# Optimization experiments

Hardware: AMD Instinct MI355X
Metric: run time of the kernel (lower is better)

## Reference

```python
import jax, jax.numpy as jnp
import numpy as np

TOP_K = 8


def setup_inputs() -> dict:
    key = jax.random.key(0)
    k1, k2 = jax.random.split(key)
    hidden_states = jax.random.normal(k1, (4, 4096, 4096), dtype=jnp.float32)
    weight = jax.random.normal(k2, (64, 4096), dtype=jnp.float32) * 0.02
    return {"hidden_states": hidden_states, "weight": weight}


def reference(hidden_states, weight):
    # Flatten [B, S, H] -> [T, H]; gating math is done in float32 (matches .float()).
    h = hidden_states.shape[-1]
    x = hidden_states.reshape(-1, h).astype(jnp.float32)
    # Router logits: [T, E] = [T, H] @ [H, E]
    logits = jnp.einsum('th,eh->te', x, weight.astype(jnp.float32))
    scores = jax.nn.softmax(logits, axis=-1)
    # Top-k expert selection (greedy router)
    topk_weight, topk_idx = jax.lax.top_k(scores, TOP_K)  # [T, K], [T, K]
    # Normalize top-k probabilities (norm_topk_prob=True)
    denom = jnp.sum(topk_weight, axis=-1, keepdims=True) + 1e-20
    topk_weight = topk_weight / denom
    return topk_weight, topk_idx
```

## Files before the change

kernel.cpp:

```cpp
#include <hip/hip_runtime.h>
#include <math.h>

typedef float  f32x4  __attribute__((ext_vector_type(4)));
typedef int    i32x4  __attribute__((ext_vector_type(4)));

#define H      4096
#define E      64
#define TOPK   8
#define TILE_T 32
#define CK     256
#define MS     4
#define NCH    16

__global__ __launch_bounds__(256)
void prep_w(const float* __restrict__ Wg, signed char* __restrict__ Wb)
{
  int n = blockIdx.x * 256 + threadIdx.x;
  int kgrp = n & 3, m = (n >> 2) & 63, e = n >> 8;
  const float* wp = Wg + e * 4096 + m * 64 + kgrp * 16;
  signed char lb[5][16];
  #pragma unroll
  for (int s = 0; s < 16; ++s) {
    long long v = (long long)rint((double)wp[s] * 2199023255552.0);
    #pragma unroll
    for (int j = 0; j < 4; ++j) {
      signed char b = (signed char)(v & 0xff);
      lb[j][s] = b;
      v = (v - b) >> 8;
    }
    lb[4][s] = (signed char)v;
  }
  int lanei = (kgrp << 4) | (e & 15);
  int eq = e >> 4;
  #pragma unroll
  for (int j = 0; j < 5; ++j) {
    i32x4 d;
    #pragma unroll
    for (int r = 0; r < 4; ++r)
      d[r] = (lb[j][4*r] & 0xFF) | ((lb[j][4*r+1] & 0xFF) << 8)
           | ((lb[j][4*r+2] & 0xFF) << 16) | ((lb[j][4*r+3] & 0xFF) << 24);
    *(i32x4*)(Wb + (((size_t)(m * 4 + eq) * 5 + j) << 10) + lanei * 16) = d;
  }
}

__global__ __launch_bounds__(64)
void comp_w(const float* __restrict__ Wg, double* __restrict__ compT)
{
  int e = blockIdx.x;
  int lane = threadIdx.x;
  double s = 0.0;
  #pragma unroll 4
  for (int i = 0; i < 64; ++i)
    s += rint((double)Wg[e * 4096 + i * 64 + lane] * 2199023255552.0);
  #pragma unroll
  for (int off = 32; off >= 1; off >>= 1)
    s += __shfl_xor(s, off);
  if (lane == 0) compT[e] = 8421504.0 * s;
}

__global__ __launch_bounds__(256)
void moe_gate_i8(const float* __restrict__ X, const signed char* __restrict__ Wb,
                 const double* __restrict__ compT, float* __restrict__ out,
                 int n_tokens)
{
  __shared__ char sm[65536];
  double* Ls = (double*)sm;

  const int tid  = threadIdx.x;
  const int lane = tid & 63;
  const int w    = tid >> 6;
  const int t0   = blockIdx.x * TILE_T;
  const int l15  = lane & 15;
  const int kg   = lane >> 4;
  const int dA   = l15 & 7;

  i32x4 z = {0, 0, 0, 0};
  int lab = l15 * 0x01010101;
  i32x4 onev = {0x01010101, 0x01010101, 0x01010101, 0x01010101};
  i32x4 labv = {lab, lab, lab, lab};
  i32x4 pr = __builtin_amdgcn_mfma_i32_16x16x64_i8(labv, onev, z, 0, 0, 0);
  i32x4 pc = __builtin_amdgcn_mfma_i32_16x16x64_i8(onev, labv, z, 0, 0, 0);
  int qrow[4], qcol[4];
  #pragma unroll
  for (int r = 0; r < 4; ++r) { qrow[r] = pr[r] >> 6; qcol[r] = pc[r] >> 6; }

  i32x4 aA3 = z, aA4 = z, aA5 = z, aA6 = z, aA7 = z;
  i32x4 aB3 = z, aB4 = z, aB5 = z, aB6 = z, aB7 = z;

  const signed char* bpp = Wb + w * 5120 + lane * 16;

  #define STAGE(c_, buf_)                                                     \
  {                                                                           \
    _Pragma("unroll")                                                         \
    for (int q = 0; q < 8; ++q) {                                             \
      const int tok_ = w * 8 + q;                                             \
      const float* src_ = X + (size_t)(t0 + tok_) * H + (c_) * CK             \
                            + ((lane ^ (tok_ & 7)) << 2);                     \
      char* dst_ = sm + ((buf_) << 15) + (tok_ << 10);                        \
      __builtin_amdgcn_global_load_lds(                                       \
          (const __attribute__((address_space(1))) void*)src_,                \
          (__attribute__((address_space(3))) void*)dst_, 16, 0, 0);           \
    }                                                                         \
  }

  #define CONV4(xv, W0, W1, W2, W3)                                           \
  {                                                                           \
    unsigned w32[16];                                                         \
    _Pragma("unroll")                                                         \
    for (int r = 0; r < 4; ++r) {                                             \
      f32x4 t_ = xv[r];                                                       \
      _Pragma("unroll")                                                       \
      for (int jj = 0; jj < 4; ++jj)                                          \
        w32[r*4+jj] = ((unsigned)(int)(t_[jj] * 268435456.0f)) ^ 0x00808080u; \
    }                                                                         \
    _Pragma("unroll")                                                         \
    for (int r = 0; r < 4; ++r) {                                             \
      unsigned u0 = w32[4*r], u1 = w32[4*r+1], u2 = w32[4*r+2], u3 = w32[4*r+3];\
      unsigned p01, p23;                                                      \
      p01 = __builtin_amdgcn_perm(u1, u0, 0x04000400u);                       \
      p23 = __builtin_amdgcn_perm(u3, u2, 0x04000400u);                       \
      W0[r] = (int)__builtin_amdgcn_perm(p23, p01, 0x05040100u);              \
      p01 = __builtin_amdgcn_perm(u1, u0, 0x05010501u);                       \
      p23 = __builtin_amdgcn_perm(u3, u2, 0x05010501u);                       \
      W1[r] = (int)__builtin_amdgcn_perm(p23, p01, 0x05040100u);              \
      p01 = __builtin_amdgcn_perm(u1, u0, 0x06020602u);                       \
      p23 = __builtin_amdgcn_perm(u3, u2, 0x06020602u);                       \
      W2[r] = (int)__builtin_amdgcn_perm(p23, p01, 0x05040100u);              \
      p01 = __builtin_amdgcn_perm(u1, u0, 0x07030703u);                       \
      p23 = __builtin_amdgcn_perm(u3, u2, 0x07030703u);                       \
      W3[r] = (int)__builtin_amdgcn_perm(p23, p01, 0x05040100u);              \
    }                                                                         \
  }

  STAGE(0, 0);
  __syncthreads();

  for (int c = 0; c < NCH; ++c) {
    const int cur = c & 1;

    i32x4 bf[4][5];
    #pragma unroll
    for (int m = 0; m < MS; ++m)
      #pragma unroll
      for (int j = 0; j < 5; ++j)
        bf[m][j] = *(const i32x4*)(bpp + (size_t)m * 20480 + (j << 10));
    bpp += (size_t)MS * 20480;

    if (c < NCH - 1) STAGE(c + 1, cur ^ 1);

    const char* base = sm + (cur << 15);
    #pragma unroll
    for (int m = 0; m < MS; ++m) {
      f32x4 va[4], vb[4];
      #pragma unroll
      for (int j = 0; j < 4; ++j) {
        const int slot = ((m * 16 + kg * 4 + j) ^ dA) << 4;
        va[j] = *(const f32x4*)(base + (l15 << 10) + slot);
        vb[j] = *(const f32x4*)(base + ((l15 + 16) << 10) + slot);
      }
      i32x4 xA0, xA1, xA2, xA3, xB0, xB1, xB2, xB3;
      CONV4(va, xA0, xA1, xA2, xA3);
      CONV4(vb, xB0, xB1, xB2, xB3);
      i32x4 b0 = bf[m][0], b1 = bf[m][1], b2 = bf[m][2], b3 = bf[m][3], b4 = bf[m][4];
      aA3 = __builtin_amdgcn_mfma_i32_16x16x64_i8(xA0, b3, aA3, 0, 0, 0);
      aB3 = __builtin_amdgcn_mfma_i32_16x16x64_i8(xB0, b3, aB3, 0, 0, 0);
      aA4 = __builtin_amdgcn_mfma_i32_16x16x64_i8(xA0, b4, aA4, 0, 0, 0);
      aB4 = __builtin_amdgcn_mfma_i32_16x16x64_i8(xB0, b4, aB4, 0, 0, 0);
      aA5 = __builtin_amdgcn_mfma_i32_16x16x64_i8(xA1, b4, aA5, 0, 0, 0);
      aB5 = __builtin_amdgcn_mfma_i32_16x16x64_i8(xB1, b4, aB5, 0, 0, 0);
      aA6 = __builtin_amdgcn_mfma_i32_16x16x64_i8(xA2, b4, aA6, 0, 0, 0);
      aB6 = __builtin_amdgcn_mfma_i32_16x16x64_i8(xB2, b4, aB6, 0, 0, 0);
      aA7 = __builtin_amdgcn_mfma_i32_16x16x64_i8(xA3, b4, aA7, 0, 0, 0);
      aB7 = __builtin_amdgcn_mfma_i32_16x16x64_i8(xB3, b4, aB7, 0, 0, 0);
      aA3 = __builtin_amdgcn_mfma_i32_16x16x64_i8(xA1, b2, aA3, 0, 0, 0);
      aB3 = __builtin_amdgcn_mfma_i32_16x16x64_i8(xB1, b2, aB3, 0, 0, 0);
      aA4 = __builtin_amdgcn_mfma_i32_16x16x64_i8(xA1, b3, aA4, 0, 0, 0);
      aB4 = __builtin_amdgcn_mfma_i32_16x16x64_i8(xB1, b3, aB4, 0, 0, 0);
      aA5 = __builtin_amdgcn_mfma_i32_16x16x64_i8(xA2, b3, aA5, 0, 0, 0);
      aB5 = __builtin_amdgcn_mfma_i32_16x16x64_i8(xB2, b3, aB5, 0, 0, 0);
      aA6 = __builtin_amdgcn_mfma_i32_16x16x64_i8(xA3, b3, aA6, 0, 0, 0);
      aB6 = __builtin_amdgcn_mfma_i32_16x16x64_i8(xB3, b3, aB6, 0, 0, 0);
      aA3 = __builtin_amdgcn_mfma_i32_16x16x64_i8(xA2, b1, aA3, 0, 0, 0);
      aB3 = __builtin_amdgcn_mfma_i32_16x16x64_i8(xB2, b1, aB3, 0, 0, 0);
      aA4 = __builtin_amdgcn_mfma_i32_16x16x64_i8(xA2, b2, aA4, 0, 0, 0);
      aB4 = __builtin_amdgcn_mfma_i32_16x16x64_i8(xB2, b2, aB4, 0, 0, 0);
      aA5 = __builtin_amdgcn_mfma_i32_16x16x64_i8(xA3, b2, aA5, 0, 0, 0);
      aB5 = __builtin_amdgcn_mfma_i32_16x16x64_i8(xB3, b2, aB5, 0, 0, 0);
      aA3 = __builtin_amdgcn_mfma_i32_16x16x64_i8(xA3, b0, aA3, 0, 0, 0);
      aB3 = __builtin_amdgcn_mfma_i32_16x16x64_i8(xB3, b0, aB3, 0, 0, 0);
      aA4 = __builtin_amdgcn_mfma_i32_16x16x64_i8(xA3, b1, aA4, 0, 0, 0);
      aB4 = __builtin_amdgcn_mfma_i32_16x16x64_i8(xB3, b1, aB4, 0, 0, 0);
    }

    __syncthreads();
  }
  #undef STAGE
  #undef CONV4

  #pragma unroll
  for (int r = 0; r < 4; ++r) {
    int ex = w * 16 + qcol[r];
    double pA = (16777216.0          * (double)aA3[r]
               + 4294967296.0        * (double)aA4[r]
               + 1099511627776.0     * (double)aA5[r]
               + 281474976710656.0   * (double)aA6[r]
               + 72057594037927936.0 * (double)aA7[r]
               + compT[ex]) * 1.6940658945086007e-21;
    double pB = (16777216.0          * (double)aB3[r]
               + 4294967296.0        * (double)aB4[r]
               + 1099511627776.0     * (double)aB5[r]
               + 281474976710656.0   * (double)aB6[r]
               + 72057594037927936.0 * (double)aB7[r]
               + compT[ex]) * 1.6940658945086007e-21;
    Ls[qrow[r] * E + ex]        = pA;
    Ls[(16 + qrow[r]) * E + ex] = pB;
  }
  __syncthreads();

  for (int tt2 = 0; tt2 < 8; tt2++) {
    int t = w * 8 + tt2;
    double val = Ls[t * E + lane];

    double mx = val;
    #pragma unroll
    for (int off = 32; off >= 1; off >>= 1)
      mx = fmax(mx, __shfl_xor(mx, off));

    float p = expf((float)(val - mx));
    float S = p;
    #pragma unroll
    for (int off = 32; off >= 1; off >>= 1)
      S += __shfl_xor(S, off);

    double cur = val;
    float myw = 0.f; int myidx = 0;
    float psum = 0.f;
    #pragma unroll
    for (int r = 0; r < TOPK; r++) {
      double v = cur; int ii = lane;
      #pragma unroll
      for (int off = 32; off >= 1; off >>= 1) {
        double ov = __shfl_xor(v, off);
        int    oi = __shfl_xor(ii, off);
        if (ov > v || (ov == v && oi < ii)) { v = ov; ii = oi; }
      }
      float pw = __shfl(p, ii);
      psum += pw;
      if (lane == r) { myw = pw; myidx = ii; }
      if (lane == ii) cur = -INFINITY;
    }
    float denom = psum + 1e-20f * S;
    if (lane < TOPK) {
      size_t gt = (size_t)(t0 + t);
      out[gt * TOPK + lane] = myw / denom;
      out[(size_t)n_tokens * TOPK + gt * TOPK + lane] = (float)myidx;
    }
  }
}

extern "C" void kernel_launch(void* const* d_in, const int* in_sizes, int n_in,
                              void* d_out, int out_size, void* d_ws, size_t ws_size,
                              hipStream_t stream)
{
  const float* X  = (const float*)d_in[0];
  const float* Wg = (const float*)d_in[1];
  float* out = (float*)d_out;
  signed char* Wb = (signed char*)d_ws;
  double* compT   = (double*)((char*)d_ws + 1310720);
  int n_tokens = in_sizes[0] / H;

  prep_w<<<64, 256, 0, stream>>>(Wg, Wb);
  comp_w<<<64, 64, 0, stream>>>(Wg, compT);
  moe_gate_i8<<<n_tokens / TILE_T, 256, 0, stream>>>(X, Wb, compT, out, n_tokens);
}
```

Baseline: 144.9 us.

## Convert X to int8 planes once at staging instead of per-wave in compute loop

Result: faster. 135.8 us (-6.3%).

```diff
diff --git a/kernel.cpp b/kernel.cpp
--- a/kernel.cpp
+++ b/kernel.cpp
@@ -63,8 +63,8 @@
                  const double* __restrict__ compT, float* __restrict__ out,
                  int n_tokens)
 {
-  __shared__ char sm[65536];
-  double* Ls = (double*)sm;
+  __shared__ char As[65536];
+  double* Ls = (double*)As;
 
   const int tid  = threadIdx.x;
   const int lane = tid & 63;
@@ -72,7 +72,6 @@
   const int t0   = blockIdx.x * TILE_T;
   const int l15  = lane & 15;
   const int kg   = lane >> 4;
-  const int dA   = l15 & 7;
 
   i32x4 z = {0, 0, 0, 0};
   int lab = l15 * 0x01010101;
@@ -87,57 +86,53 @@
   i32x4 aA3 = z, aA4 = z, aA5 = z, aA6 = z, aA7 = z;
   i32x4 aB3 = z, aB4 = z, aB5 = z, aB6 = z, aB7 = z;
 
+  const int kgrp = lane >> 2;
+  const int wrd  = lane & 3;
+  const int swzs = ((lane >> 3) & 7) << 4;
+  const float* xbase = X + (size_t)t0 * H + lane * 4;
+
   const signed char* bpp = Wb + w * 5120 + lane * 16;
 
-  #define STAGE(c_, buf_)                                                     \
+  f32x4 xr[8];
+
+  #define CONVWRITE(boff_)                                                    \
   {                                                                           \
     _Pragma("unroll")                                                         \
     for (int q = 0; q < 8; ++q) {                                             \
-      const int tok_ = w * 8 + q;                                             \
-      const float* src_ = X + (size_t)(t0 + tok_) * H + (c_) * CK             \
-                            + ((lane ^ (tok_ & 7)) << 2);                     \
-      char* dst_ = sm + ((buf_) << 15) + (tok_ << 10);                        \
-      __builtin_amdgcn_global_load_lds(                                       \
-          (const __attribute__((address_space(1))) void*)src_,                \
-          (__attribute__((address_space(3))) void*)dst_, 16, 0, 0);           \
-    }                                                                         \
-  }
-
-  #define CONV4(xv, W0, W1, W2, W3)                                           \
-  {                                                                           \
-    unsigned w32[16];                                                         \
-    _Pragma("unroll")                                                         \
-    for (int r = 0; r < 4; ++r) {                                             \
-      f32x4 t_ = xv[r];                                                       \
-      _Pragma("unroll")                                                       \
-      for (int jj = 0; jj < 4; ++jj)                                          \
-        w32[r*4+jj] = ((unsigned)(int)(t_[jj] * 268435456.0f)) ^ 0x00808080u; \
-    }                                                                         \
-    _Pragma("unroll")                                                         \
-    for (int r = 0; r < 4; ++r) {                                             \
-      unsigned u0 = w32[4*r], u1 = w32[4*r+1], u2 = w32[4*r+2], u3 = w32[4*r+3];\
-      unsigned p01, p23;                                                      \
+      const int r = w * 8 + q;                                                \
+      unsigned u0 = ((unsigned)(int)(xr[q][0] * 268435456.0f)) ^ 0x00808080u; \
+      unsigned u1 = ((unsigned)(int)(xr[q][1] * 268435456.0f)) ^ 0x00808080u; \
+      unsigned u2 = ((unsigned)(int)(xr[q][2] * 268435456.0f)) ^ 0x00808080u; \
+      unsigned u3 = ((unsigned)(int)(xr[q][3] * 268435456.0f)) ^ 0x00808080u; \
+      unsigned p01, p23, W0, W1, W2, W3;                                      \
       p01 = __builtin_amdgcn_perm(u1, u0, 0x04000400u);                       \
       p23 = __builtin_amdgcn_perm(u3, u2, 0x04000400u);                       \
-      W0[r] = (int)__builtin_amdgcn_perm(p23, p01, 0x05040100u);              \
+      W0  = __builtin_amdgcn_perm(p23, p01, 0x05040100u);                     \
       p01 = __builtin_amdgcn_perm(u1, u0, 0x05010501u);                       \
       p23 = __builtin_amdgcn_perm(u3, u2, 0x05010501u);                       \
-      W1[r] = (int)__builtin_amdgcn_perm(p23, p01, 0x05040100u);              \
+      W1  = __builtin_amdgcn_perm(p23, p01, 0x05040100u);                     \
       p01 = __builtin_amdgcn_perm(u1, u0, 0x06020602u);                       \
       p23 = __builtin_amdgcn_perm(u3, u2, 0x06020602u);                       \
-      W2[r] = (int)__builtin_amdgcn_perm(p23, p01, 0x05040100u);              \
+      W2  = __builtin_amdgcn_perm(p23, p01, 0x05040100u);                     \
       p01 = __builtin_amdgcn_perm(u1, u0, 0x07030703u);                       \
       p23 = __builtin_amdgcn_perm(u3, u2, 0x07030703u);                       \
-      W3[r] = (int)__builtin_amdgcn_perm(p23, p01, 0x05040100u);              \
+      W3  = __builtin_amdgcn_perm(p23, p01, 0x05040100u);                     \
+      char* base = As + (boff_) + (kgrp << 11) + (((r << 4) ^ swzs))          \
+                 + (wrd << 2);                                                \
+      *(unsigned*)(base + 0x000) = W0;                                        \
+      *(unsigned*)(base + 0x200) = W1;                                        \
+      *(unsigned*)(base + 0x400) = W2;                                        \
+      *(unsigned*)(base + 0x600) = W3;                                        \
     }                                                                         \
   }
 
-  STAGE(0, 0);
+  #pragma unroll
+  for (int q = 0; q < 8; ++q)
+    xr[q] = *(const f32x4*)(xbase + (size_t)(w * 8 + q) * H);
+  CONVWRITE(0);
   __syncthreads();
 
   for (int c = 0; c < NCH; ++c) {
-    const int cur = c & 1;
-
     i32x4 bf[4][5];
     #pragma unroll
     for (int m = 0; m < MS; ++m)
@@ -145,57 +140,67 @@
       for (int j = 0; j < 5; ++j)
         bf[m][j] = *(const i32x4*)(bpp + (size_t)m * 20480 + (j << 10));
     bpp += (size_t)MS * 20480;
-
-    if (c < NCH - 1) STAGE(c + 1, cur ^ 1);
-
-    const char* base = sm + (cur << 15);
-    #pragma unroll
-    for (int m = 0; m < MS; ++m) {
-      f32x4 va[4], vb[4];
-      #pragma unroll
-      for (int j = 0; j < 4; ++j) {
-        const int slot = ((m * 16 + kg * 4 + j) ^ dA) << 4;
-        va[j] = *(const f32x4*)(base + (l15 << 10) + slot);
-        vb[j] = *(const f32x4*)(base + ((l15 + 16) << 10) + slot);
+    __builtin_amdgcn_sched_barrier(0);
+
+    if (c < NCH - 1) {
+      #pragma unroll
+      for (int q = 0; q < 8; ++q)
+        xr[q] = *(const f32x4*)(xbase + (size_t)(w * 8 + q) * H + (c + 1) * CK);
+    }
+    __builtin_amdgcn_sched_barrier(0);
+
+    {
+      const char* base_ = As + ((c & 1) << 15);
+      #pragma unroll
+      for (int m = 0; m < MS; ++m) {
+        const int kq   = 4 * m + kg;
+        const int swzr = ((kq >> 1) & 7) << 4;
+        const char* abase = base_ + (kq << 11) + (((l15 << 4) ^ swzr));
+        i32x4 b0 = bf[m][0], b1 = bf[m][1], b2 = bf[m][2];
+        i32x4 b3 = bf[m][3], b4 = bf[m][4];
+        i32x4 xA0 = *(const i32x4*)(abase + 0x000);
+        i32x4 xA1 = *(const i32x4*)(abase + 0x200);
+        i32x4 xA2 = *(const i32x4*)(abase + 0x400);
+        i32x4 xA3 = *(const i32x4*)(abase + 0x600);
+        i32x4 xB0 = *(const i32x4*)(abase + 0x100);
+        i32x4 xB1 = *(const i32x4*)(abase + 0x300);
+        i32x4 xB2 = *(const i32x4*)(abase + 0x500);
+        i32x4 xB3 = *(const i32x4*)(abase + 0x700);
+        aA3 = __builtin_amdgcn_mfma_i32_16x16x64_i8(xA0, b3, aA3, 0, 0, 0);
+        aB3 = __builtin_amdgcn_mfma_i32_16x16x64_i8(xB0, b3, aB3, 0, 0, 0);
+        aA4 = __builtin_amdgcn_mfma_i32_16x16x64_i8(xA0, b4, aA4, 0, 0, 0);
+        aB4 = __builtin_amdgcn_mfma_i32_16x16x64_i8(xB0, b4, aB4, 0, 0, 0);
+        aA5 = __builtin_amdgcn_mfma_i32_16x16x64_i8(xA1, b4, aA5, 0, 0, 0);
+        aB5 = __builtin_amdgcn_mfma_i32_16x16x64_i8(xB1, b4, aB5, 0, 0, 0);
+        aA6 = __builtin_amdgcn_mfma_i32_16x16x64_i8(xA2, b4, aA6, 0, 0, 0);
+        aB6 = __builtin_amdgcn_mfma_i32_16x16x64_i8(xB2, b4, aB6, 0, 0, 0);
+        aA7 = __builtin_amdgcn_mfma_i32_16x16x64_i8(xA3, b4, aA7, 0, 0, 0);
+        aB7 = __builtin_amdgcn_mfma_i32_16x16x64_i8(xB3, b4, aB7, 0, 0, 0);
+        aA3 = __builtin_amdgcn_mfma_i32_16x16x64_i8(xA1, b2, aA3, 0, 0, 0);
+        aB3 = __builtin_amdgcn_mfma_i32_16x16x64_i8(xB1, b2, aB3, 0, 0, 0);
+        aA4 = __builtin_amdgcn_mfma_i32_16x16x64_i8(xA1, b3, aA4, 0, 0, 0);
+        aB4 = __builtin_amdgcn_mfma_i32_16x16x64_i8(xB1, b3, aB4, 0, 0, 0);
+        aA5 = __builtin_amdgcn_mfma_i32_16x16x64_i8(xA2, b3, aA5, 0, 0, 0);
+        aB5 = __builtin_amdgcn_mfma_i32_16x16x64_i8(xB2, b3, aB5, 0, 0, 0);
+        aA6 = __builtin_amdgcn_mfma_i32_16x16x64_i8(xA3, b3, aA6, 0, 0, 0);
+        aB6 = __builtin_amdgcn_mfma_i32_16x16x64_i8(xB3, b3, aB6, 0, 0, 0);
+        aA3 = __builtin_amdgcn_mfma_i32_16x16x64_i8(xA2, b1, aA3, 0, 0, 0);
+        aB3 = __builtin_amdgcn_mfma_i32_16x16x64_i8(xB2, b1, aB3, 0, 0, 0);
+        aA4 = __builtin_amdgcn_mfma_i32_16x16x64_i8(xA2, b2, aA4, 0, 0, 0);
+        aB4 = __builtin_amdgcn_mfma_i32_16x16x64_i8(xB2, b2, aB4, 0, 0, 0);
+        aA5 = __builtin_amdgcn_mfma_i32_16x16x64_i8(xA3, b2, aA5, 0, 0, 0);
+        aB5 = __builtin_amdgcn_mfma_i32_16x16x64_i8(xB3, b2, aB5, 0, 0, 0);
+        aA3 = __builtin_amdgcn_mfma_i32_16x16x64_i8(xA3, b0, aA3, 0, 0, 0);
+        aB3 = __builtin_amdgcn_mfma_i32_16x16x64_i8(xB3, b0, aB3, 0, 0, 0);
+        aA4 = __builtin_amdgcn_mfma_i32_16x16x64_i8(xA3, b1, aA4, 0, 0, 0);
+        aB4 = __builtin_amdgcn_mfma_i32_16x16x64_i8(xB3, b1, aB4, 0, 0, 0);
       }
-      i32x4 xA0, xA1, xA2, xA3, xB0, xB1, xB2, xB3;
-      CONV4(va, xA0, xA1, xA2, xA3);
-      CONV4(vb, xB0, xB1, xB2, xB3);
-      i32x4 b0 = bf[m][0], b1 = bf[m][1], b2 = bf[m][2], b3 = bf[m][3], b4 = bf[m][4];
-      aA3 = __builtin_amdgcn_mfma_i32_16x16x64_i8(xA0, b3, aA3, 0, 0, 0);
-      aB3 = __builtin_amdgcn_mfma_i32_16x16x64_i8(xB0, b3, aB3, 0, 0, 0);
-      aA4 = __builtin_amdgcn_mfma_i32_16x16x64_i8(xA0, b4, aA4, 0, 0, 0);
-      aB4 = __builtin_amdgcn_mfma_i32_16x16x64_i8(xB0, b4, aB4, 0, 0, 0);
-      aA5 = __builtin_amdgcn_mfma_i32_16x16x64_i8(xA1, b4, aA5, 0, 0, 0);
-      aB5 = __builtin_amdgcn_mfma_i32_16x16x64_i8(xB1, b4, aB5, 0, 0, 0);
-      aA6 = __builtin_amdgcn_mfma_i32_16x16x64_i8(xA2, b4, aA6, 0, 0, 0);
-      aB6 = __builtin_amdgcn_mfma_i32_16x16x64_i8(xB2, b4, aB6, 0, 0, 0);
-      aA7 = __builtin_amdgcn_mfma_i32_16x16x64_i8(xA3, b4, aA7, 0, 0, 0);
-      aB7 = __builtin_amdgcn_mfma_i32_16x16x64_i8(xB3, b4, aB7, 0, 0, 0);
-      aA3 = __builtin_amdgcn_mfma_i32_16x16x64_i8(xA1, b2, aA3, 0, 0, 0);
-      aB3 = __builtin_amdgcn_mfma_i32_16x16x64_i8(xB1, b2, aB3, 0, 0, 0);
-      aA4 = __builtin_amdgcn_mfma_i32_16x16x64_i8(xA1, b3, aA4, 0, 0, 0);
-      aB4 = __builtin_amdgcn_mfma_i32_16x16x64_i8(xB1, b3, aB4, 0, 0, 0);
-      aA5 = __builtin_amdgcn_mfma_i32_16x16x64_i8(xA2, b3, aA5, 0, 0, 0);
-      aB5 = __builtin_amdgcn_mfma_i32_16x16x64_i8(xB2, b3, aB5, 0, 0, 0);
-      aA6 = __builtin_amdgcn_mfma_i32_16x16x64_i8(xA3, b3, aA6, 0, 0, 0);
-      aB6 = __builtin_amdgcn_mfma_i32_16x16x64_i8(xB3, b3, aB6, 0, 0, 0);
-      aA3 = __builtin_amdgcn_mfma_i32_16x16x64_i8(xA2, b1, aA3, 0, 0, 0);
-      aB3 = __builtin_amdgcn_mfma_i32_16x16x64_i8(xB2, b1, aB3, 0, 0, 0);
-      aA4 = __builtin_amdgcn_mfma_i32_16x16x64_i8(xA2, b2, aA4, 0, 0, 0);
-      aB4 = __builtin_amdgcn_mfma_i32_16x16x64_i8(xB2, b2, aB4, 0, 0, 0);
-      aA5 = __builtin_amdgcn_mfma_i32_16x16x64_i8(xA3, b2, aA5, 0, 0, 0);
-      aB5 = __builtin_amdgcn_mfma_i32_16x16x64_i8(xB3, b2, aB5, 0, 0, 0);
-      aA3 = __builtin_amdgcn_mfma_i32_16x16x64_i8(xA3, b0, aA3, 0, 0, 0);
-      aB3 = __builtin_amdgcn_mfma_i32_16x16x64_i8(xB3, b0, aB3, 0, 0, 0);
-      aA4 = __builtin_amdgcn_mfma_i32_16x16x64_i8(xA3, b1, aA4, 0, 0, 0);
-      aB4 = __builtin_amdgcn_mfma_i32_16x16x64_i8(xB3, b1, aB4, 0, 0, 0);
-    }
-
+    }
+
+    if (c < NCH - 1) CONVWRITE(((c + 1) & 1) << 15);
     __syncthreads();
   }
-  #undef STAGE
-  #undef CONV4
+  #undef CONVWRITE
 
   #pragma unroll
   for (int r = 0; r < 4; ++r) {
```
